# Performance work log

Measured on AMD Instinct MI355X. Metric: run time of the kernel, lower is better.

The kernel has to match this reference:

```python
import jax, jax.numpy as jnp
import numpy as np

NUM_HEADS = 16
D_MODEL = 1024


def setup_inputs() -> dict:
    key = jax.random.key(0)
    ks = jax.random.split(key, 12)
    B, S, D = 2, 2048, D_MODEL
    inp = {
        "query": jax.random.normal(ks[0], (B, S, D), dtype=jnp.float32),
        "key": jax.random.normal(ks[1], (B, S, D), dtype=jnp.float32),
        "value": jax.random.normal(ks[2], (B, S, D), dtype=jnp.float32),
        "mask": jax.random.randint(ks[3], (B, 1, S), 0, 2).astype(jnp.bool_),
    }
    # Linear layer params, stored as (in, out) so y = x @ W + b
    sd = 1.0 / np.sqrt(D)
    for i, nm in enumerate(["q", "k", "v", "o"]):
        inp[f"W{nm}"] = jax.random.uniform(ks[4 + 2 * i], (D, D), jnp.float32, -sd, sd)
        inp[f"b{nm}"] = jax.random.uniform(ks[5 + 2 * i], (D,), jnp.float32, -sd, sd)
    return inp


def _split_heads(x):
    # [B, S, D] -> [B, H, S, d_k]
    B, S, D = x.shape
    return x.reshape(B, S, NUM_HEADS, D // NUM_HEADS).transpose(0, 2, 1, 3)


def reference(query, key, value, mask, Wq, bq, Wk, bk, Wv, bv, Wo, bo):
    B, Sq, D = query.shape
    d_k = D // NUM_HEADS
    scale = 1.0 / np.sqrt(d_k)

    q = _split_heads(query @ Wq + bq)   # [B,H,Sq,dk]
    k = _split_heads(key @ Wk + bk)     # [B,H,Sk,dk]
    v = _split_heads(value @ Wv + bv)   # [B,H,Sk,dk]

    scores = jnp.einsum("bhqd,bhkd->bhqk", q, k) * scale  # [B,H,Sq,Sk]
    # mask: [B,1,Sk] bool, True = masked; broadcast over heads and queries
    scores = jnp.where(mask[:, None, :, :], -jnp.inf, scores)
    attn = jax.nn.softmax(scores, axis=-1)
    attn = jnp.nan_to_num(attn, nan=0.0)  # fully-masked rows -> 0 (matches torch)

    ctx = jnp.einsum("bhqk,bhkd->bhqd", attn, v)  # [B,H,Sq,dk]
    ctx = ctx.transpose(0, 2, 1, 3).reshape(B, Sq, D)  # combine heads
    out = ctx @ Wo + bo
    return out
```

## Files before the change

### kernel.cpp

```cpp
#include <hip/hip_runtime.h>


typedef unsigned short u16;
typedef unsigned int u32;
typedef __attribute__((ext_vector_type(8))) short bf16x8;
typedef __attribute__((ext_vector_type(4))) float f32x4;
typedef __attribute__((ext_vector_type(16))) float f32x16;
typedef __attribute__((ext_vector_type(2))) int i32x2;

static __device__ __forceinline__ u16 f2bf(float x) {
  union { float f; u32 i; } v; v.f = x;
  return (u16)((v.i + 0x8000u) >> 16);
}

static __device__ __forceinline__ u32 cvtpk(float lo, float hi) {
  u32 r;
  asm("v_cvt_pk_bf16_f32 %0, %1, %2" : "=v"(r) : "v"(lo), "v"(hi));
  return r;
}

#define MFMA_B16(a, b, c) __builtin_amdgcn_mfma_f32_16x16x32_bf16((a), (b), (c), 0, 0, 0)
#define MFMA32_B16(a, b, c) __builtin_amdgcn_mfma_f32_32x32x16_bf16((a), (b), (c), 0, 0, 0)

__global__ __launch_bounds__(256) void prep_w(
    const float* __restrict__ w0, const float* __restrict__ w1,
    const float* __restrict__ w2, const float* __restrict__ w3,
    u16* __restrict__ t0, u16* __restrict__ t1,
    u16* __restrict__ t2, u16* __restrict__ t3) {
  __shared__ u16 tile[64 * 68];
  const float* W; u16* T;
  switch (blockIdx.z) {
    case 0: W = w0; T = t0; break;
    case 1: W = w1; T = t1; break;
    case 2: W = w2; T = t2; break;
    default: W = w3; T = t3; break;
  }
  const int t = threadIdx.x;
  const int k0 = blockIdx.x * 64, n0 = blockIdx.y * 64;
#pragma unroll
  for (int it = 0; it < 4; ++it) {
    int idx = it * 256 + t;
    int r = idx >> 4, c4 = idx & 15;
    float4 v = *(const float4*)&W[(size_t)(k0 + r) * 1024 + n0 + c4 * 4];
    tile[r * 68 + c4 * 4 + 0] = f2bf(v.x);
    tile[r * 68 + c4 * 4 + 1] = f2bf(v.y);
    tile[r * 68 + c4 * 4 + 2] = f2bf(v.z);
    tile[r * 68 + c4 * 4 + 3] = f2bf(v.w);
  }
  __syncthreads();
#pragma unroll
  for (int it = 0; it < 2; ++it) {
    int idx = it * 256 + t;
    int n = idx >> 3, kc = idx & 7;
    bf16x8 pk;
#pragma unroll
    for (int j = 0; j < 8; ++j) pk[j] = (short)tile[(kc * 8 + j) * 68 + n];
    *(bf16x8*)&T[(size_t)(n0 + n) * 1024 + k0 + kc * 8] = pk;
  }
}

template <int MT, int AMODE, int OMODE>
__global__ __launch_bounds__(256) void gemm_bias(
    const void* a0v, const void* a1v, const void* a2v,
    const u16* __restrict__ Wt,
    const float* b0, const float* b1, const float* b2,
    void* o0, void* o1, void* o2) {
  __shared__ __align__(16) u16 As[MT * 32 * 32];
  __shared__ __align__(16) u16 Bs[128 * 32];
  const int t = threadIdx.x, wave = t >> 6, lane = t & 63;
  const int l15 = lane & 15, quad = lane >> 4;
  const int m0 = blockIdx.x * (MT * 32);
  const int n0 = blockIdx.y * 128;
  const int rg = (OMODE == 3) ? (n0 >> 10) : 0;
  const void* Av = (rg == 0) ? a0v : (rg == 1 ? a1v : a2v);
  const float* bp = (rg == 0) ? b0 : (rg == 1 ? b1 : b2);
  const int nb = (OMODE == 3) ? (n0 & 1023) : n0;
  const int wr = (wave >> 1) * (MT * 16), wc = (wave & 1) * 64;

  const f32x4 fz = {0.f, 0.f, 0.f, 0.f};
  f32x4 acc[MT][4];
#pragma unroll
  for (int mt = 0; mt < MT; ++mt)
#pragma unroll
    for (int nt = 0; nt < 4; ++nt) acc[mt][nt] = fz;

  float4 pa[MT / 2][2]; bf16x8 pab[MT / 2]; bf16x8 pb[2];
#pragma unroll
  for (int s = 0; s < MT / 2; ++s) {
    int idx = s * 256 + t, row = idx >> 2, seg = idx & 3;
    if (AMODE == 1) {
      const float* ap = (const float*)Av + (size_t)(m0 + row) * 1024 + seg * 8;
      pa[s][0] = *(const float4*)ap; pa[s][1] = *(const float4*)(ap + 4);
    } else {
      pab[s] = *(const bf16x8*)((const u16*)Av + (size_t)(m0 + row) * 1024 + seg * 8);
    }
  }
#pragma unroll
  for (int s = 0; s < 2; ++s) {
    int idx = s * 256 + t, row = idx >> 2, seg = idx & 3;
    pb[s] = *(const bf16x8*)&Wt[(size_t)(n0 + row) * 1024 + seg * 8];
  }

  for (int kb = 0; kb < 1024; kb += 32) {
    __syncthreads();
#pragma unroll
    for (int s = 0; s < MT / 2; ++s) {
      int idx = s * 256 + t, row = idx >> 2, seg = idx & 3;
      bf16x8 pk;
      if (AMODE == 1) {
        pk[0] = (short)f2bf(pa[s][0].x); pk[1] = (short)f2bf(pa[s][0].y);
        pk[2] = (short)f2bf(pa[s][0].z); pk[3] = (short)f2bf(pa[s][0].w);
        pk[4] = (short)f2bf(pa[s][1].x); pk[5] = (short)f2bf(pa[s][1].y);
        pk[6] = (short)f2bf(pa[s][1].z); pk[7] = (short)f2bf(pa[s][1].w);
      } else pk = pab[s];
      *(bf16x8*)&As[row * 32 + seg * 8] = pk;
    }
#pragma unroll
    for (int s = 0; s < 2; ++s) {
      int idx = s * 256 + t, row = idx >> 2, seg = idx & 3;
      *(bf16x8*)&Bs[row * 32 + seg * 8] = pb[s];
    }
    __syncthreads();
    const int kn = (kb + 32) & 1023;
#pragma unroll
    for (int s = 0; s < MT / 2; ++s) {
      int idx = s * 256 + t, row = idx >> 2, seg = idx & 3;
      if (AMODE == 1) {
        const float* ap = (const float*)Av + (size_t)(m0 + row) * 1024 + kn + seg * 8;
        pa[s][0] = *(const float4*)ap; pa[s][1] = *(const float4*)(ap + 4);
      } else {
        pab[s] = *(const bf16x8*)((const u16*)Av + (size_t)(m0 + row) * 1024 + kn + seg * 8);
      }
    }
#pragma unroll
    for (int s = 0; s < 2; ++s) {
      int idx = s * 256 + t, row = idx >> 2, seg = idx & 3;
      pb[s] = *(const bf16x8*)&Wt[(size_t)(n0 + row) * 1024 + kn + seg * 8];
    }
    bf16x8 a[MT], bfr[4];
#pragma unroll
    for (int mt = 0; mt < MT; ++mt)
      a[mt] = *(const bf16x8*)&As[(wr + mt * 16 + l15) * 32 + quad * 8];
#pragma unroll
    for (int nt = 0; nt < 4; ++nt)
      bfr[nt] = *(const bf16x8*)&Bs[(wc + nt * 16 + l15) * 32 + quad * 8];
#pragma unroll
    for (int mt = 0; mt < MT; ++mt)
#pragma unroll
      for (int nt = 0; nt < 4; ++nt)
        acc[mt][nt] = MFMA_B16(a[mt], bfr[nt], acc[mt][nt]);
  }

#pragma unroll
  for (int nt = 0; nt < 4; ++nt) {
    const int n = nb + wc + nt * 16 + l15;
    const float bv = bp[n];
#pragma unroll
    for (int mt = 0; mt < MT; ++mt)
#pragma unroll
      for (int r = 0; r < 4; ++r) {
        const int m = m0 + wr + mt * 16 + quad * 4 + r;
        const float val = acc[mt][nt][r] + bv;
        if (OMODE == 2) {
          ((float*)o0)[(size_t)m * 1024 + n] = val;
        } else if (OMODE == 0) {
          ((u16*)o0)[(size_t)m * 1024 + n] = f2bf(val);
        } else {
          if (rg == 0)      ((u16*)o0)[(size_t)m * 1024 + n] = f2bf(val);
          else if (rg == 1) ((u16*)o1)[(size_t)m * 1024 + n] = f2bf(val);
          else {
            const int h = n >> 6, d = n & 63, bb = m >> 11, ss = m & 2047;
            ((u16*)o2)[((size_t)(bb * 16 + h) * 64 + d) * 2048 + ss] = f2bf(val);
          }
        }
      }
  }
}

__global__ __launch_bounds__(256) void attn_fused(
    const u16* Q, const u16* __restrict__ K,
    const u16* __restrict__ Vt, const int* __restrict__ mask,
    u16* ctx) {
  __shared__ __align__(16) u16 Ks[8 * 128 * 8];
  __shared__ __align__(16) u16 Vs[16 * 64 * 8];
  __shared__ float Lw[4][32];
  const int t = threadIdx.x, wave = t >> 6, lane = t & 63;
  const int l31 = lane & 31, hi = lane >> 5;
  const int bh = blockIdx.y, b = bh >> 4, h = bh & 15;
  const int q0w = blockIdx.x * 128 + wave * 32;
  const float cs = 0.125f * 1.44269504f;

  const u16* Qp2 = Q + (size_t)(b * 2048 + q0w) * 1024 + h * 64;
  bf16x8 qb[4];
#pragma unroll
  for (int kd = 0; kd < 4; ++kd)
    qb[kd] = *(const bf16x8*)(Qp2 + (size_t)l31 * 1024 + kd * 16 + hi * 8);

  const u16* Kbase = K + (size_t)(b * 2048) * 1024 + h * 64;
  const u16* Vbase = Vt + (size_t)bh * 64 * 2048;

  bf16x8 gk[4], gv[4];
#pragma unroll
  for (int s = 0; s < 4; ++s) {
    int slot = s * 256 + t;
    int kr = slot >> 3, ksg = slot & 7;
    gk[s] = *(const bf16x8*)&Kbase[(size_t)kr * 1024 + ksg * 8];
    int vr = slot >> 4, vsg = slot & 15;
    gv[s] = *(const bf16x8*)&Vbase[(size_t)vr * 2048 + vsg * 8];
  }
  int mk0 = mask[b * 2048 + lane];
  int mk1 = mask[b * 2048 + 64 + lane];

  const f32x16 sz = {0.f};
  f32x16 o0a = sz, o1a = sz;
  float lsum = 0.f;
  const int hs = hi * 4;

  for (int kt = 0; kt < 2048; kt += 128) {
    __syncthreads();
#pragma unroll
    for (int s = 0; s < 4; ++s) {
      int slot = s * 256 + t;
      int kr = slot >> 3, ksg = slot & 7;
      *(bf16x8*)&Ks[ksg * 1024 + ((kr ^ (ksg & 7)) * 8)] = gk[s];
      int vr = slot >> 4, vsg = slot & 15;
      *(bf16x8*)&Vs[vsg * 512 + ((vr ^ (vsg & 7)) * 8)] = gv[s];
    }
    const unsigned long long mb0 = __ballot(mk0 == 0);
    const unsigned long long mb1 = __ballot(mk1 == 0);
    const u32 mw[4] = {(u32)mb0, (u32)(mb0 >> 32), (u32)mb1, (u32)(mb1 >> 32)};
    __syncthreads();
    const int kn = (kt + 128) & 2047;
#pragma unroll
    for (int s = 0; s < 4; ++s) {
      int slot = s * 256 + t;
      int kr = slot >> 3, ksg = slot & 7;
      gk[s] = *(const bf16x8*)&Kbase[(size_t)(kn + kr) * 1024 + ksg * 8];
      int vr = slot >> 4, vsg = slot & 15;
      gv[s] = *(const bf16x8*)&Vbase[(size_t)vr * 2048 + kn + vsg * 8];
    }
    mk0 = mask[b * 2048 + kn + lane];
    mk1 = mask[b * 2048 + kn + 64 + lane];

#pragma unroll
    for (int kg = 0; kg < 4; ++kg) {
      f32x16 S = sz;
#pragma unroll
      for (int kd = 0; kd < 4; ++kd) {
        const int dseg = kd * 2 + hi;
        const bf16x8 kf = *(const bf16x8*)
            &Ks[dseg * 1024 + (((kg * 32 + l31) ^ (dseg & 7)) * 8)];
        S = MFMA32_B16(kf, qb[kd], S);
      }
      const u32 mws = mw[kg] >> hs;
      u32 W[8];
      float p[16];
#pragma unroll
      for (int c = 0; c < 4; ++c) {
#pragma unroll
        for (int j = 0; j < 4; ++j) {
          float pv = exp2f(S[c * 4 + j] * cs);
          pv = __int_as_float(__float_as_int(pv) &
                              (-(int)((mws >> (8 * c + j)) & 1u)));
          p[c * 4 + j] = pv;
          lsum += pv;
        }
        W[2 * c + 0] = cvtpk(p[c * 4 + 0], p[c * 4 + 1]);
        W[2 * c + 1] = cvtpk(p[c * 4 + 2], p[c * 4 + 3]);
      }
      {
        i32x2 r0 = __builtin_amdgcn_permlane32_swap((int)W[0], (int)W[2], false, false);
        i32x2 r1 = __builtin_amdgcn_permlane32_swap((int)W[1], (int)W[3], false, false);
        i32x2 r2 = __builtin_amdgcn_permlane32_swap((int)W[4], (int)W[6], false, false);
        i32x2 r3 = __builtin_amdgcn_permlane32_swap((int)W[5], (int)W[7], false, false);
        union { bf16x8 v; u32 w[4]; } pa0, pa1;
        pa0.w[0] = (u32)r0[0]; pa0.w[1] = (u32)r1[0];
        pa0.w[2] = (u32)r0[1]; pa0.w[3] = (u32)r1[1];
        pa1.w[0] = (u32)r2[0]; pa1.w[1] = (u32)r3[0];
        pa1.w[2] = (u32)r2[1]; pa1.w[3] = (u32)r3[1];
#pragma unroll
        for (int ks2 = 0; ks2 < 2; ++ks2) {
          const bf16x8 pav = ks2 ? pa1.v : pa0.v;
          const int kseg = (kg * 2 + ks2) * 2 + hi;
          const bf16x8 vf0 = *(const bf16x8*)
              &Vs[kseg * 512 + ((l31 ^ (kseg & 7)) * 8)];
          const bf16x8 vf1 = *(const bf16x8*)
              &Vs[kseg * 512 + (((32 + l31) ^ (kseg & 7)) * 8)];
          o0a = MFMA32_B16(pav, vf0, o0a);
          o1a = MFMA32_B16(pav, vf1, o1a);
        }
      }
    }
  }
  lsum += __shfl_xor(lsum, 32);
  {
    const float inv = lsum > 0.f ? 1.f / lsum : 0.f;
    if (hi == 0) Lw[wave][l31] = inv;
  }
  u16* cp = ctx + (size_t)(b * 2048 + q0w) * 1024 + h * 64;
#pragma unroll
  for (int c = 0; c < 4; ++c) {
    const float4 iv4 = *(const float4*)&Lw[wave][c * 8 + hi * 4];
#pragma unroll
    for (int j = 0; j < 4; ++j) {
      const int row = 8 * c + 4 * hi + j;
      const float iv = (&iv4.x)[j];
      cp[(size_t)row * 1024 + l31]      = f2bf(o0a[c * 4 + j] * iv);
      cp[(size_t)row * 1024 + 32 + l31] = f2bf(o1a[c * 4 + j] * iv);
    }
  }
}

extern "C" void kernel_launch(void* const* d_in, const int* in_sizes, int n_in,
                              void* d_out, int out_size, void* d_ws, size_t ws_size,
                              hipStream_t stream) {
  const float* q    = (const float*)d_in[0];
  const float* k    = (const float*)d_in[1];
  const float* v    = (const float*)d_in[2];
  const int*   mask = (const int*)d_in[3];
  const float* Wq = (const float*)d_in[4];  const float* bq = (const float*)d_in[5];
  const float* Wk = (const float*)d_in[6];  const float* bk = (const float*)d_in[7];
  const float* Wv = (const float*)d_in[8];  const float* bv = (const float*)d_in[9];
  const float* Wo = (const float*)d_in[10]; const float* bo = (const float*)d_in[11];

  char* ws = (char*)d_ws;
  u16*   Kp  = (u16*)(ws + ((size_t)0 << 20));
  u16*   Vt  = (u16*)(ws + ((size_t)8 << 20));
  float* O32 = (float*)ws;

  char* od = (char*)d_out;
  u16* ctx = (u16*)od;
  u16* WqT = (u16*)(od + ((size_t)8 << 20));
  u16* WkT = (u16*)(od + ((size_t)10 << 20));
  u16* WvT = (u16*)(od + ((size_t)12 << 20));
  u16* WoT = (u16*)(od + ((size_t)14 << 20));

  dim3 blk(256);
  prep_w<<<dim3(16, 16, 4), blk, 0, stream>>>(Wq, Wk, Wv, Wo, WqT, WkT, WvT, WoT);
  gemm_bias<4, 1, 3><<<dim3(32, 24), blk, 0, stream>>>(
      q, k, v, WqT, bq, bk, bv, (void*)ctx, (void*)Kp, (void*)Vt);
  attn_fused<<<dim3(16, 32), dim3(256), 0, stream>>>(ctx, Kp, Vt, mask, ctx);
  gemm_bias<2, 0, 2><<<dim3(64, 8), blk, 0, stream>>>(
      ctx, nullptr, nullptr, WoT, bo, nullptr, nullptr, (void*)O32, nullptr, nullptr);
  hipMemcpyAsync(d_out, O32, (size_t)out_size * sizeof(float),
                 hipMemcpyDeviceToDevice, stream);
}
```

Baseline: 265.0 us.

## Split attention key range across wave pairs and reduce partial outputs in LDS

```diff
diff --git a/kernel.cpp b/kernel.cpp
--- a/kernel.cpp
+++ b/kernel.cpp
@@ -181,13 +181,18 @@
     const u16* Q, const u16* __restrict__ K,
     const u16* __restrict__ Vt, const int* __restrict__ mask,
     u16* ctx) {
-  __shared__ __align__(16) u16 Ks[8 * 128 * 8];
-  __shared__ __align__(16) u16 Vs[16 * 64 * 8];
-  __shared__ float Lw[4][32];
+  __shared__ __align__(16) u16 SMEM[16384];
+  __shared__ float Lw[2][32];
+  __shared__ float Ls[2][32];
+  u16* Ks = SMEM;
+  u16* Vs = SMEM + 8192;
+  float* scratch = (float*)SMEM;
+
   const int t = threadIdx.x, wave = t >> 6, lane = t & 63;
   const int l31 = lane & 31, hi = lane >> 5;
+  const int qh = wave & 1, kh = wave >> 1;
   const int bh = blockIdx.y, b = bh >> 4, h = bh & 15;
-  const int q0w = blockIdx.x * 128 + wave * 32;
+  const int q0w = blockIdx.x * 64 + qh * 32;
   const float cs = 0.125f * 1.44269504f;
 
   const u16* Qp2 = Q + (size_t)(b * 2048 + q0w) * 1024 + h * 64;
@@ -208,8 +213,7 @@
     int vr = slot >> 4, vsg = slot & 15;
     gv[s] = *(const bf16x8*)&Vbase[(size_t)vr * 2048 + vsg * 8];
   }
-  int mk0 = mask[b * 2048 + lane];
-  int mk1 = mask[b * 2048 + 64 + lane];
+  int mk = mask[b * 2048 + kh * 64 + lane];
 
   const f32x16 sz = {0.f};
   f32x16 o0a = sz, o1a = sz;
@@ -226,9 +230,8 @@
       int vr = slot >> 4, vsg = slot & 15;
       *(bf16x8*)&Vs[vsg * 512 + ((vr ^ (vsg & 7)) * 8)] = gv[s];
     }
-    const unsigned long long mb0 = __ballot(mk0 == 0);
-    const unsigned long long mb1 = __ballot(mk1 == 0);
-    const u32 mw[4] = {(u32)mb0, (u32)(mb0 >> 32), (u32)mb1, (u32)(mb1 >> 32)};
+    const unsigned long long mb = __ballot(mk == 0);
+    const u32 mw[2] = {(u32)mb, (u32)(mb >> 32)};
     __syncthreads();
     const int kn = (kt + 128) & 2047;
 #pragma unroll
@@ -239,17 +242,17 @@
       int vr = slot >> 4, vsg = slot & 15;
       gv[s] = *(const bf16x8*)&Vbase[(size_t)vr * 2048 + kn + vsg * 8];
     }
-    mk0 = mask[b * 2048 + kn + lane];
-    mk1 = mask[b * 2048 + kn + 64 + lane];
-
-#pragma unroll
-    for (int kg = 0; kg < 4; ++kg) {
+    mk = mask[b * 2048 + kn + kh * 64 + lane];
+
+#pragma unroll
+    for (int kg = 0; kg < 2; ++kg) {
+      const int kga = kh * 2 + kg;
       f32x16 S = sz;
 #pragma unroll
       for (int kd = 0; kd < 4; ++kd) {
         const int dseg = kd * 2 + hi;
         const bf16x8 kf = *(const bf16x8*)
-            &Ks[dseg * 1024 + (((kg * 32 + l31) ^ (dseg & 7)) * 8)];
+            &Ks[dseg * 1024 + (((kga * 32 + l31) ^ (dseg & 7)) * 8)];
         S = MFMA32_B16(kf, qb[kd], S);
       }
       const u32 mws = mw[kg] >> hs;
@@ -281,7 +284,7 @@
 #pragma unroll
         for (int ks2 = 0; ks2 < 2; ++ks2) {
           const bf16x8 pav = ks2 ? pa1.v : pa0.v;
-          const int kseg = (kg * 2 + ks2) * 2 + hi;
+          const int kseg = (kga * 2 + ks2) * 2 + hi;
           const bf16x8 vf0 = *(const bf16x8*)
               &Vs[kseg * 512 + ((l31 ^ (kseg & 7)) * 8)];
           const bf16x8 vf1 = *(const bf16x8*)
@@ -293,20 +296,39 @@
     }
   }
   lsum += __shfl_xor(lsum, 32);
-  {
+
+  __syncthreads();
+  if (kh == 1) {
+    float* dst = scratch + qh * 2048;
+#pragma unroll
+    for (int e = 0; e < 16; ++e) {
+      dst[e * 64 + lane] = o0a[e];
+      dst[(16 + e) * 64 + lane] = o1a[e];
+    }
+    if (hi == 0) Ls[qh][l31] = lsum;
+  }
+  __syncthreads();
+  if (kh == 0) {
+    const float* src = scratch + qh * 2048;
+#pragma unroll
+    for (int e = 0; e < 16; ++e) {
+      o0a[e] += src[e * 64 + lane];
+      o1a[e] += src[(16 + e) * 64 + lane];
+    }
+    lsum += Ls[qh][l31];
     const float inv = lsum > 0.f ? 1.f / lsum : 0.f;
-    if (hi == 0) Lw[wave][l31] = inv;
-  }
-  u16* cp = ctx + (size_t)(b * 2048 + q0w) * 1024 + h * 64;
-#pragma unroll
-  for (int c = 0; c < 4; ++c) {
-    const float4 iv4 = *(const float4*)&Lw[wave][c * 8 + hi * 4];
-#pragma unroll
-    for (int j = 0; j < 4; ++j) {
-      const int row = 8 * c + 4 * hi + j;
-      const float iv = (&iv4.x)[j];
-      cp[(size_t)row * 1024 + l31]      = f2bf(o0a[c * 4 + j] * iv);
-      cp[(size_t)row * 1024 + 32 + l31] = f2bf(o1a[c * 4 + j] * iv);
+    if (hi == 0) Lw[qh][l31] = inv;
+    u16* cp = ctx + (size_t)(b * 2048 + q0w) * 1024 + h * 64;
+#pragma unroll
+    for (int c = 0; c < 4; ++c) {
+      const float4 iv4 = *(const float4*)&Lw[qh][c * 8 + hi * 4];
+#pragma unroll
+      for (int j = 0; j < 4; ++j) {
+        const int row = 8 * c + 4 * hi + j;
+        const float iv = (&iv4.x)[j];
+        cp[(size_t)row * 1024 + l31]      = f2bf(o0a[c * 4 + j] * iv);
+        cp[(size_t)row * 1024 + 32 + l31] = f2bf(o1a[c * 4 + j] * iv);
+      }
     }
   }
 }
@@ -339,7 +361,7 @@
   prep_w<<<dim3(16, 16, 4), blk, 0, stream>>>(Wq, Wk, Wv, Wo, WqT, WkT, WvT, WoT);
   gemm_bias<4, 1, 3><<<dim3(32, 24), blk, 0, stream>>>(
       q, k, v, WqT, bq, bk, bv, (void*)ctx, (void*)Kp, (void*)Vt);
-  attn_fused<<<dim3(16, 32), dim3(256), 0, stream>>>(ctx, Kp, Vt, mask, ctx);
+  attn_fused<<<dim3(32, 32), dim3(256), 0, stream>>>(ctx, Kp, Vt, mask, ctx);
   gemm_bias<2, 0, 2><<<dim3(64, 8), blk, 0, stream>>>(
       ctx, nullptr, nullptr, WoT, bo, nullptr, nullptr, (void*)O32, nullptr, nullptr);
   hipMemcpyAsync(d_out, O32, (size_t)out_size * sizeof(float),
```

Result: slower. 277.8 us (+4.8%).

## Compute softmax row sums via MFMA with ones and apply mask as additive bias

Applied to the files above, without the earlier changes.

```diff
diff --git a/kernel.cpp b/kernel.cpp
--- a/kernel.cpp
+++ b/kernel.cpp
@@ -183,7 +183,7 @@
     u16* ctx) {
   __shared__ __align__(16) u16 Ks[8 * 128 * 8];
   __shared__ __align__(16) u16 Vs[16 * 64 * 8];
-  __shared__ float Lw[4][32];
+  __shared__ __align__(16) float Mf[128];
   const int t = threadIdx.x, wave = t >> 6, lane = t & 63;
   const int l31 = lane & 31, hi = lane >> 5;
   const int bh = blockIdx.y, b = bh >> 4, h = bh & 15;
@@ -208,13 +208,15 @@
     int vr = slot >> 4, vsg = slot & 15;
     gv[s] = *(const bf16x8*)&Vbase[(size_t)vr * 2048 + vsg * 8];
   }
-  int mk0 = mask[b * 2048 + lane];
-  int mk1 = mask[b * 2048 + 64 + lane];
+  int gmv = mask[b * 2048 + (t & 127)];
+
+  bf16x8 onesb;
+#pragma unroll
+  for (int j = 0; j < 8; ++j) onesb[j] = (short)0x3F80;
 
   const f32x16 sz = {0.f};
   f32x16 o0a = sz, o1a = sz;
-  float lsum = 0.f;
-  const int hs = hi * 4;
+  f32x16 osum = sz;
 
   for (int kt = 0; kt < 2048; kt += 128) {
     __syncthreads();
@@ -226,9 +228,7 @@
       int vr = slot >> 4, vsg = slot & 15;
       *(bf16x8*)&Vs[vsg * 512 + ((vr ^ (vsg & 7)) * 8)] = gv[s];
     }
-    const unsigned long long mb0 = __ballot(mk0 == 0);
-    const unsigned long long mb1 = __ballot(mk1 == 0);
-    const u32 mw[4] = {(u32)mb0, (u32)(mb0 >> 32), (u32)mb1, (u32)(mb1 >> 32)};
+    if (t < 128) Mf[t] = gmv ? -__builtin_inff() : 0.f;
     __syncthreads();
     const int kn = (kt + 128) & 2047;
 #pragma unroll
@@ -239,8 +239,7 @@
       int vr = slot >> 4, vsg = slot & 15;
       gv[s] = *(const bf16x8*)&Vbase[(size_t)vr * 2048 + kn + vsg * 8];
     }
-    mk0 = mask[b * 2048 + kn + lane];
-    mk1 = mask[b * 2048 + kn + 64 + lane];
+    gmv = mask[b * 2048 + kn + (t & 127)];
 
 #pragma unroll
     for (int kg = 0; kg < 4; ++kg) {
@@ -252,21 +251,16 @@
             &Ks[dseg * 1024 + (((kg * 32 + l31) ^ (dseg & 7)) * 8)];
         S = MFMA32_B16(kf, qb[kd], S);
       }
-      const u32 mws = mw[kg] >> hs;
       u32 W[8];
-      float p[16];
 #pragma unroll
       for (int c = 0; c < 4; ++c) {
-#pragma unroll
-        for (int j = 0; j < 4; ++j) {
-          float pv = exp2f(S[c * 4 + j] * cs);
-          pv = __int_as_float(__float_as_int(pv) &
-                              (-(int)((mws >> (8 * c + j)) & 1u)));
-          p[c * 4 + j] = pv;
-          lsum += pv;
-        }
-        W[2 * c + 0] = cvtpk(p[c * 4 + 0], p[c * 4 + 1]);
-        W[2 * c + 1] = cvtpk(p[c * 4 + 2], p[c * 4 + 3]);
+        const float4 bias4 = *(const float4*)&Mf[kg * 32 + c * 8 + hi * 4];
+        const float p0 = exp2f(fmaf(S[c * 4 + 0], cs, bias4.x));
+        const float p1 = exp2f(fmaf(S[c * 4 + 1], cs, bias4.y));
+        const float p2 = exp2f(fmaf(S[c * 4 + 2], cs, bias4.z));
+        const float p3 = exp2f(fmaf(S[c * 4 + 3], cs, bias4.w));
+        W[2 * c + 0] = cvtpk(p0, p1);
+        W[2 * c + 1] = cvtpk(p2, p3);
       }
       {
         i32x2 r0 = __builtin_amdgcn_permlane32_swap((int)W[0], (int)W[2], false, false);
@@ -288,25 +282,21 @@
               &Vs[kseg * 512 + (((32 + l31) ^ (kseg & 7)) * 8)];
           o0a = MFMA32_B16(pav, vf0, o0a);
           o1a = MFMA32_B16(pav, vf1, o1a);
+          osum = MFMA32_B16(pav, onesb, osum);
         }
       }
     }
   }
-  lsum += __shfl_xor(lsum, 32);
-  {
-    const float inv = lsum > 0.f ? 1.f / lsum : 0.f;
-    if (hi == 0) Lw[wave][l31] = inv;
-  }
   u16* cp = ctx + (size_t)(b * 2048 + q0w) * 1024 + h * 64;
 #pragma unroll
   for (int c = 0; c < 4; ++c) {
-    const float4 iv4 = *(const float4*)&Lw[wave][c * 8 + hi * 4];
 #pragma unroll
     for (int j = 0; j < 4; ++j) {
+      const int e = c * 4 + j;
       const int row = 8 * c + 4 * hi + j;
-      const float iv = (&iv4.x)[j];
-      cp[(size_t)row * 1024 + l31]      = f2bf(o0a[c * 4 + j] * iv);
-      cp[(size_t)row * 1024 + 32 + l31] = f2bf(o1a[c * 4 + j] * iv);
+      const float iv = osum[e] > 0.f ? 1.f / osum[e] : 0.f;
+      cp[(size_t)row * 1024 + l31]      = f2bf(o0a[e] * iv);
+      cp[(size_t)row * 1024 + 32 + l31] = f2bf(o1a[e] * iv);
     }
   }
 }
```

New measurement: 259.8 us. 1.02x faster.
